# Performance work log

Hardware: AMD Instinct MI355X
Metric: run time of the kernel (lower is better)

## Reference

```python
import jax, jax.numpy as jnp
from jax import lax
import numpy as np

CONF_THRESH = 0.015
NMS_DIST = 4
BORDER = 4
RED = 8


def setup_inputs() -> dict:
    key = jax.random.key(0)
    k1, k2, k3, k4, k5 = jax.random.split(key, 5)
    B, C, H, W = 32, 128, 64, 64
    MID, NCLS = 256, RED * RED + 1
    return {
        "x": jax.random.normal(k1, (B, C, H, W), dtype=jnp.float32),
        "w1": jax.random.normal(k2, (MID, C, 3, 3), dtype=jnp.float32) * 0.05,
        "b1": jax.random.normal(k3, (MID,), dtype=jnp.float32) * 0.05,
        "w2": jax.random.normal(k4, (NCLS, MID, 1, 1), dtype=jnp.float32) * 0.05,
        "b2": jax.random.normal(k5, (NCLS,), dtype=jnp.float32) * 0.05,
    }


def _conv3x3(x, w, b):
    y = lax.conv_general_dilated(
        x, w, window_strides=(1, 1), padding="SAME",
        dimension_numbers=("NCHW", "OIHW", "NCHW"))
    return y + b[None, :, None, None]


def _max_pool(s, r):
    # s: [B, H, W]; infinity-norm neighborhood max, window (2r+1)x(2r+1)
    return lax.reduce_window(
        s, -jnp.inf, lax.max,
        window_dimensions=(1, 2 * r + 1, 2 * r + 1),
        window_strides=(1, 1, 1), padding="SAME")


def _grid_nms(scores, r, iters=8):
    # Iterated local-max suppression; converges to the greedy (sorted-by-score)
    # grid NMS of the original nms_fast routine for distinct scores.
    zeros = jnp.zeros_like(scores)
    max_mask = (scores == _max_pool(scores, r)) & (scores > 0)
    for _ in range(iters):
        supp = _max_pool(max_mask.astype(scores.dtype), r) > 0
        supp_scores = jnp.where(supp, zeros, scores)
        new_max = (supp_scores == _max_pool(supp_scores, r)) & (supp_scores > 0)
        max_mask = max_mask | (new_max & ~supp)
    return jnp.where(max_mask, scores, zeros)


def reference(x, w1, b1, w2, b2):
    B, _, hh, ww = x.shape
    h = jax.nn.relu(_conv3x3(x, w1, b1))                       # [B, mid, hh, ww]
    semi = jnp.einsum("bchw,oc->bohw", h, w2[:, :, 0, 0]) + b2[None, :, None, None]
    dense = jax.nn.softmax(semi, axis=1)                        # [B, 65, hh, ww]
    nodust = dense[:, :-1]                                      # drop dust bin
    # depth-to-space: [B,64,hh,ww] -> [B, hh*8, ww*8]
    heat = nodust.transpose(0, 2, 3, 1).reshape(B, hh, ww, RED, RED)
    heat = heat.transpose(0, 1, 3, 2, 4).reshape(B, hh * RED, ww * RED)
    # confidence threshold
    scores = jnp.where(heat >= CONF_THRESH, heat, 0.0)
    # grid-based NMS (dense keep-map formulation of nms_fast)
    kept = _grid_nms(scores, NMS_DIST)
    # border removal
    Hi, Wi = hh * RED, ww * RED
    yy = jnp.arange(Hi)
    xx = jnp.arange(Wi)
    border = ((yy[:, None] >= BORDER) & (yy[:, None] < Hi - BORDER) &
              (xx[None, :] >= BORDER) & (xx[None, :] < Wi - BORDER))
    return kept * border[None, :, :].astype(kept.dtype)
```

## Files before the change

kernel.cpp:

```cpp
#include <hip/hip_runtime.h>
#include <hip/hip_bf16.h>
#include <stdint.h>

#define BATCH 32
#define CIN 128
#define HH 64
#define WW 64
#define MID 256
#define NCLS 65
#define HI 512
#define NWORDS 8
#define HBS2 264
#define SEMS 68

typedef _Float16 half8 __attribute__((ext_vector_type(8)));
typedef _Float16 half4v __attribute__((ext_vector_type(4)));
typedef _Float16 half2v __attribute__((ext_vector_type(2)));
typedef float f32x4 __attribute__((ext_vector_type(4)));

__global__ __launch_bounds__(256) void prep_w1f(
    const float* __restrict__ w1, _Float16* __restrict__ w1fh,
    _Float16* __restrict__ w1fl)
{
    const int idx = blockIdx.x * 256 + threadIdx.x;
    const int j = idx & 7, lane = (idx >> 3) & 63, mt = (idx >> 9) & 15;
    const int s = (idx >> 13) & 3, kix = idx >> 15;
    const int m = mt * 16 + (lane & 15);
    const int c = s * 32 + (lane >> 4) * 8 + j;
    const int ky = kix / 3, kx = kix - ky * 3;
    const float v = w1[((m * CIN + c) * 3 + ky) * 3 + kx];
    const _Float16 hi = (_Float16)v;
    w1fh[idx] = hi;
    w1fl[idx] = (_Float16)(v - (float)hi);
}

__global__ __launch_bounds__(256) void prep_w2f(
    const float* __restrict__ w2, _Float16* __restrict__ w2fh,
    _Float16* __restrict__ w2fl)
{
    const int idx = blockIdx.x * 256 + threadIdx.x;
    const int j = idx & 7, lane = (idx >> 3) & 63;
    const int ks = (idx >> 9) & 7, mt = idx >> 12;
    const int o = mt * 16 + (lane & 15);
    const int k = ks * 32 + (lane >> 4) * 8 + j;
    const float v = (o < NCLS) ? w2[o * MID + k] : 0.f;
    const _Float16 hi = (_Float16)v;
    w2fh[idx] = hi;
    w2fl[idx] = (_Float16)(v - (float)hi);
}

__global__ __launch_bounds__(256, 3) void head_kernel(
    const float* __restrict__ x,
    const _Float16* __restrict__ w1fh, const _Float16* __restrict__ w1fl,
    const _Float16* __restrict__ w2fh, const _Float16* __restrict__ w2fl,
    const float* __restrict__ b1, const float* __restrict__ b2,
    float* __restrict__ out)
{
    const int b  = blockIdx.z;
    const int y0 = blockIdx.y * 8, x0 = blockIdx.x * 8;
    const int tid = threadIdx.x;
    const int lane = tid & 63, w = tid >> 6;
    const int n = lane & 15, q = lane >> 4;

    __shared__ __align__(16) unsigned char SM[51200];
    char* const xhb = (char*)SM;
    _Float16* const hbh = (_Float16*)SM;
    _Float16* const hbl = hbh + 32 * HBS2;
    float* const sem  = (float*)(SM + 33792);
    float* const rinv = sem + 32 * SEMS;

    const float* xb = x + (size_t)b * CIN * HH * WW;
    for (int i = tid; i < 6400; i += 256) {
        const int c2 = i / 100, pos = i - c2 * 100;
        const int r = pos / 10, cc = pos - r * 10;
        const int gy = y0 - 1 + r, gx = x0 - 1 + cc;
        float v0 = 0.f, v1 = 0.f;
        if ((unsigned)gy < HH && (unsigned)gx < WW) {
            const float* p = xb + (c2 * 2 * HH + gy) * WW + gx;
            v0 = p[0]; v1 = p[HH * WW];
        }
        const _Float16 h0 = (_Float16)v0, h1 = (_Float16)v1;
        half2v hi = {h0, h1};
        half2v lo = {(_Float16)(v0 - (float)h0), (_Float16)(v1 - (float)h1)};
        const int slot = (c2 >> 2) ^ (pos & 15);
        char* p16 = xhb + pos * 256 + (slot << 4) + (c2 & 3) * 4;
        *(half2v*)p16 = hi;
        *(half2v*)(p16 + 25600) = lo;
    }
    __syncthreads();

    f32x4 acc[4][4];
#pragma unroll
    for (int i = 0; i < 4; ++i)
#pragma unroll
        for (int t = 0; t < 4; ++t) acc[i][t] = (f32x4){0.f, 0.f, 0.f, 0.f};

    int bposT[4];
#pragma unroll
    for (int t = 0; t < 4; ++t)
        bposT[t] = (t * 2 + (n >> 3)) * 10 + (n & 7);

    for (int kix = 0; kix < 9; ++kix) {
        const int ky = kix / 3;
        const int koff = ky * 10 + (kix - ky * 3);
#pragma unroll
        for (int s = 0; s < 4; ++s) {
            half8 Bh[4], Bl[4];
#pragma unroll
            for (int t = 0; t < 4; ++t) {
                const int pos = bposT[t] + koff;
                const int byteoff = pos * 256 +
                    ((((s << 2) + q) ^ (pos & 15)) << 4);
                Bh[t] = *(const half8*)(xhb + byteoff);
                Bl[t] = *(const half8*)(xhb + 25600 + byteoff);
            }
#pragma unroll
            for (int i = 0; i < 4; ++i) {
                const size_t o = (size_t)(kix * 4 + s) * 8192 +
                                 (w * 4 + i) * 512 + lane * 8;
                const half8 Ah = *(const half8*)(w1fh + o);
                const half8 Al = *(const half8*)(w1fl + o);
#pragma unroll
                for (int t = 0; t < 4; ++t) {
                    acc[i][t] = __builtin_amdgcn_mfma_f32_16x16x32_f16(
                        Ah, Bh[t], acc[i][t], 0, 0, 0);
                    acc[i][t] = __builtin_amdgcn_mfma_f32_16x16x32_f16(
                        Ah, Bl[t], acc[i][t], 0, 0, 0);
                    acc[i][t] = __builtin_amdgcn_mfma_f32_16x16x32_f16(
                        Al, Bh[t], acc[i][t], 0, 0, 0);
                }
            }
        }
    }
    __syncthreads();

    for (int hf = 0; hf < 2; ++hf) {
        if (hf) __syncthreads();
#pragma unroll
        for (int i = 0; i < 4; ++i)
#pragma unroll
            for (int tt = 0; tt < 2; ++tt) {
                const int t = hf * 2 + tt;
                const int p = tt * 16 + n;
                const int m0 = w * 64 + i * 16 + q * 4;
                const f32x4 a = acc[i][t];
                const float4 bv = *(const float4*)(b1 + m0);
                const float h0 = fmaxf(a[0] + bv.x, 0.f);
                const float h1 = fmaxf(a[1] + bv.y, 0.f);
                const float h2 = fmaxf(a[2] + bv.z, 0.f);
                const float h3 = fmaxf(a[3] + bv.w, 0.f);
                half4v hh = {(_Float16)h0, (_Float16)h1,
                             (_Float16)h2, (_Float16)h3};
                half4v hl = {(_Float16)(h0 - (float)hh[0]),
                             (_Float16)(h1 - (float)hh[1]),
                             (_Float16)(h2 - (float)hh[2]),
                             (_Float16)(h3 - (float)hh[3])};
                *(half4v*)(hbh + p * HBS2 + m0) = hh;
                *(half4v*)(hbl + p * HBS2 + m0) = hl;
            }
        __syncthreads();
        {
            const int nt = w & 1;
            const int mt0 = (w < 2) ? 0 : 3;
            const int nmt = (w < 2) ? 3 : 2;
            const int pb = nt * 16 + n;
            f32x4 a2[3];
#pragma unroll
            for (int j = 0; j < 3; ++j) a2[j] = (f32x4){0.f, 0.f, 0.f, 0.f};
#pragma unroll
            for (int ks = 0; ks < 8; ++ks) {
                const int ad = pb * HBS2 + ks * 32 + q * 8;
                const half8 B2h = *(const half8*)(hbh + ad);
                const half8 B2l = *(const half8*)(hbl + ad);
#pragma unroll
                for (int j = 0; j < 3; ++j)
                    if (j < nmt) {
                        const size_t o = (size_t)((mt0 + j) * 8 + ks) * 512 +
                                         lane * 8;
                        const half8 A2h = *(const half8*)(w2fh + o);
                        const half8 A2l = *(const half8*)(w2fl + o);
                        a2[j] = __builtin_amdgcn_mfma_f32_16x16x32_f16(
                            A2h, B2h, a2[j], 0, 0, 0);
                        a2[j] = __builtin_amdgcn_mfma_f32_16x16x32_f16(
                            A2h, B2l, a2[j], 0, 0, 0);
                        a2[j] = __builtin_amdgcn_mfma_f32_16x16x32_f16(
                            A2l, B2h, a2[j], 0, 0, 0);
                    }
            }
#pragma unroll
            for (int j = 0; j < 3; ++j)
                if (j < nmt) {
                    const int o0 = (mt0 + j) * 16 + q * 4;
#pragma unroll
                    for (int r2 = 0; r2 < 4; ++r2) {
                        const int o = o0 + r2;
                        if (o < NCLS)
                            sem[pb * SEMS + o] = a2[j][r2] + b2[o];
                    }
                }
        }
        __syncthreads();
        if (tid < 128) {
            const int p = tid >> 2, q4 = tid & 3;
            const int o0 = q4 * 17;
            const int o1 = (o0 + 17 < NCLS) ? o0 + 17 : NCLS;
            float mx = -1e30f;
            for (int o = o0; o < o1; ++o)
                mx = fmaxf(mx, sem[p * SEMS + o]);
            mx = fmaxf(mx, __shfl_xor(mx, 1));
            mx = fmaxf(mx, __shfl_xor(mx, 2));
            float ssum = 0.f;
            for (int o = o0; o < o1; ++o) {
                float e = __expf(sem[p * SEMS + o] - mx);
                sem[p * SEMS + o] = e;
                ssum += e;
            }
            ssum += __shfl_xor(ssum, 1);
            ssum += __shfl_xor(ssum, 2);
            if (q4 == 0) rinv[p] = 1.f / ssum;
        }
        __syncthreads();
        for (int t2 = tid; t2 < 2048; t2 += 256) {
            const int p = t2 >> 6, o = t2 & 63;
            float v = sem[p * SEMS + o] * rinv[p];
            if (!(v >= 0.015f)) v = 0.f;
            const int P = hf * 32 + p;
            const int py = P >> 3, px = P & 7;
            const int row = (y0 + py) * 8 + (o >> 3);
            const int col = (x0 + px) * 8 + (o & 7);
            out[((size_t)b * HI + row) * HI + col] = v;
        }
    }
}

__global__ __launch_bounds__(256) void nms_iter(
    const float* __restrict__ S, const uint64_t* __restrict__ Min,
    uint64_t* __restrict__ Mout)
{
    const int b = blockIdx.z;
    const int bx = blockIdx.x;
    const int ty = blockIdx.y * 64, tx = bx * 64;
    const int tid = threadIdx.x;

    __shared__ uint64_t smw[80 * 3];
    __shared__ uint64_t hd[80 * 3];
    __shared__ uint64_t sup[72 * 3];
    __shared__ __align__(16) float sfl[72 * 76];
    __shared__ __align__(16) float rm[40 * 64];

    if (tid < 240) {
        const int i = tid / 3, j = tid % 3;
        const int yy = ty - 8 + i;
        const int wj = bx - 1 + j;
        uint64_t v = 0;
        if (Min && (unsigned)yy < HI && (unsigned)wj < NWORDS)
            v = Min[((size_t)b * HI + yy) * NWORDS + wj];
        smw[tid] = v;
    }
    __syncthreads();
    if (tid < 240) {
        const int i = tid / 3, j = tid % 3;
        const uint64_t c = smw[i * 3 + j];
        const uint64_t l = j > 0 ? smw[i * 3 + j - 1] : 0ull;
        const uint64_t r = j < 2 ? smw[i * 3 + j + 1] : 0ull;
        uint64_t d = c;
#pragma unroll
        for (int s = 1; s <= 4; ++s)
            d |= (c >> s) | (r << (64 - s)) | (c << s) | (l >> (64 - s));
        hd[tid] = d;
    }
    __syncthreads();
    if (tid < 216) {
        const int r = tid / 3, j = tid % 3;
        uint64_t v = 0;
#pragma unroll
        for (int k = 0; k < 9; ++k) v |= hd[(r + k) * 3 + j];
        sup[tid] = v;
    }
    __syncthreads();
    const float* Sb = S + (size_t)b * HI * HI;
    for (int k = tid; k < 72 * 18; k += 256) {
        const int r = k / 18, f4 = k % 18;
        const int gy = ty - 4 + r;
        const int gx0 = tx - 4 + f4 * 4;
        float4 v = make_float4(0.f, 0.f, 0.f, 0.f);
        float* pv = (float*)&v;
        if ((unsigned)gy < HI) {
            if (gx0 >= 0 && gx0 + 3 < HI)
                v = *(const float4*)(Sb + (size_t)gy * HI + gx0);
            else {
#pragma unroll
                for (int cc = 0; cc < 4; ++cc)
                    if ((unsigned)(gx0 + cc) < HI)
                        pv[cc] = Sb[(size_t)gy * HI + gx0 + cc];
            }
        }
        const int rel64 = 60 + 4 * f4;
        const uint64_t w = sup[r * 3 + (rel64 >> 6)];
        const int b0 = rel64 & 63;
#pragma unroll
        for (int cc = 0; cc < 4; ++cc)
            if ((w >> (b0 + cc)) & 1ull) pv[cc] = 0.f;
        *(float4*)(sfl + r * 76 + f4 * 4) = v;
    }
    __syncthreads();

    for (int half = 0; half < 2; ++half) {
        const int rbase = half * 32;
        for (int k = tid; k < 40 * 16; k += 256) {
            const int rr = k / 16, x4 = (k % 16) * 4;
            const int r = rbase + rr;
            const float4 a  = *(const float4*)(sfl + r * 76 + x4);
            const float4 bq = *(const float4*)(sfl + r * 76 + x4 + 4);
            const float4 cq = *(const float4*)(sfl + r * 76 + x4 + 8);
            const float v0=a.x,v1=a.y,v2=a.z,v3=a.w;
            const float v4=bq.x,v5=bq.y,v6=bq.z,v7=bq.w;
            const float v8=cq.x,v9=cq.y,v10=cq.z,v11=cq.w;
            const float m4567 = fmaxf(fmaxf(v4,v5), fmaxf(v6,v7));
            const float m23 = fmaxf(v2,v3), m89 = fmaxf(v8,v9);
            const float o0 = fmaxf(fmaxf(fmaxf(v0,v1), m23), fmaxf(m4567, v8));
            const float o1 = fmaxf(fmaxf(v1, m23), fmaxf(m4567, m89));
            const float o2 = fmaxf(fmaxf(m23, m4567), fmaxf(m89, v10));
            const float o3 = fmaxf(fmaxf(v3, m4567), fmaxf(fmaxf(m89, v10), v11));
            *(float4*)(rm + rr * 64 + x4) = make_float4(o0,o1,o2,o3);
        }
        __syncthreads();
        {
            const int wv = tid >> 6, lane = tid & 63;
            const int rb = wv * 8;
            const int ybase = rbase + rb;
            float ring[9];
#pragma unroll
            for (int k = 0; k < 8; ++k) ring[k] = rm[(rb + k) * 64 + lane];
#pragma unroll
            for (int qq = 0; qq < 8; ++qq) {
                const int y = ybase + qq;
                ring[(qq + 8) % 9] = rm[(rb + qq + 8) * 64 + lane];
                float mv = ring[0];
#pragma unroll
                for (int k = 1; k < 9; ++k) mv = fmaxf(mv, ring[k]);
                const float c = sfl[(y + 4) * 76 + lane + 4];
                const uint64_t oldw = smw[(y + 8) * 3 + 1];
                const bool keep = ((oldw >> lane) & 1ull) || (c == mv && c > 0.f);
                const uint64_t word = __ballot(keep);
                if (lane == 0)
                    Mout[((size_t)b * HI + ty + y) * NWORDS + bx] = word;
            }
        }
        __syncthreads();
    }
}

__global__ __launch_bounds__(256) void finalize_bits(
    float* __restrict__ S, const uint64_t* __restrict__ Mw)
{
    const int i4 = blockIdx.x * 256 + threadIdx.x;
    const size_t base = (size_t)i4 * 4;
    const int x = (int)(base & 511);
    const int y = (int)((base >> 9) & 511);
    const int bb = (int)(base >> 18);
    const uint64_t w = Mw[((size_t)bb * HI + y) * NWORDS + (x >> 6)];
    float4 v = ((const float4*)S)[i4];
    float* pv = (float*)&v;
    const bool rowok = (y >= 4) && (y < HI - 4);
#pragma unroll
    for (int cc = 0; cc < 4; ++cc) {
        const int xx = x + cc;
        const bool keep = rowok && (xx >= 4) && (xx < HI - 4) &&
                          ((w >> (xx & 63)) & 1ull);
        if (!keep) pv[cc] = 0.f;
    }
    ((float4*)S)[i4] = v;
}

extern "C" void kernel_launch(void* const* d_in, const int* in_sizes, int n_in,
                              void* d_out, int out_size, void* d_ws, size_t ws_size,
                              hipStream_t stream) {
    const float* x  = (const float*)d_in[0];
    const float* w1 = (const float*)d_in[1];
    const float* b1 = (const float*)d_in[2];
    const float* w2 = (const float*)d_in[3];
    const float* b2 = (const float*)d_in[4];
    float* out = (float*)d_out;

    char* wsb = (char*)d_ws;
    _Float16* w1fh = (_Float16*)(wsb);
    _Float16* w1fl = (_Float16*)(wsb + 0x90000);
    _Float16* w2fh = (_Float16*)(wsb + 0x120000);
    _Float16* w2fl = (_Float16*)(wsb + 0x130000);
    uint64_t* MA   = (uint64_t*)(wsb + 0x140000);
    uint64_t* MB   = (uint64_t*)(wsb + 0x240000);

    prep_w1f<<<294912 / 256, 256, 0, stream>>>(w1, w1fh, w1fl);
    prep_w2f<<<20480 / 256, 256, 0, stream>>>(w2, w2fh, w2fl);
    head_kernel<<<dim3(8, 8, BATCH), 256, 0, stream>>>(
        x, w1fh, w1fl, w2fh, w2fl, b1, b2, out);

    dim3 g(NWORDS, 8, BATCH);
    nms_iter<<<g, 256, 0, stream>>>(out, nullptr, MA);
    for (int it = 0; it < 4; ++it) {
        nms_iter<<<g, 256, 0, stream>>>(out, MA, MB);
        nms_iter<<<g, 256, 0, stream>>>(out, MB, MA);
    }
    const int nf4 = BATCH * HI * HI / 4;
    finalize_bits<<<nf4 / 256, 256, 0, stream>>>(out, MA);
}
```

Before: 532.4 us.

## Fuse pairs of NMS iterations into one kernel with halo recompute

Adds an nms_pair kernel that performs two suppression iterations per launch. It loads a wider halo tile, computes the intermediate keep mask in shared memory over an enlarged region, then runs the second iteration on the inner tile. The launch sequence drops from nine nms_iter launches to four nms_pair launches plus one nms_iter. This halves global reads of scores and mask words and cuts launch overhead, in exchange for redundant halo computation and more shared memory per block.

```diff
diff --git a/kernel.cpp b/kernel.cpp
--- a/kernel.cpp
+++ b/kernel.cpp
@@ -351,6 +351,240 @@
     }
 }
 
+__global__ __launch_bounds__(256) void nms_pair(
+    const float* __restrict__ S, const uint64_t* __restrict__ Min,
+    uint64_t* __restrict__ Mout)
+{
+    const int b = blockIdx.z;
+    const int bx = blockIdx.x;
+    const int ty = blockIdx.y * 64, tx = bx * 64;
+    const int tid = threadIdx.x;
+
+    __shared__ uint64_t smw[96 * 3];
+    __shared__ uint64_t hd[96 * 3];
+    __shared__ uint64_t sup[88 * 3];
+    __shared__ __align__(16) float sfl[88 * 88];
+    __shared__ __align__(16) float hm[28 * 80];
+    __shared__ uint64_t mkA[80 * 3];
+
+    for (int k = tid; k < 288; k += 256) {
+        const int i = k / 3, j = k - (k / 3) * 3;
+        const int yy = ty - 16 + i;
+        const int wj = bx - 1 + j;
+        uint64_t v = 0;
+        if (Min && (unsigned)yy < HI && (unsigned)wj < NWORDS)
+            v = Min[((size_t)b * HI + yy) * NWORDS + wj];
+        smw[k] = v;
+    }
+    __syncthreads();
+    for (int k = tid; k < 288; k += 256) {
+        const int j = k % 3;
+        const uint64_t c = smw[k];
+        const uint64_t l = j > 0 ? smw[k - 1] : 0ull;
+        const uint64_t r = j < 2 ? smw[k + 1] : 0ull;
+        uint64_t d = c;
+#pragma unroll
+        for (int s = 1; s <= 4; ++s)
+            d |= (c >> s) | (r << (64 - s)) | (c << s) | (l >> (64 - s));
+        hd[k] = d;
+    }
+    __syncthreads();
+    for (int k = tid; k < 264; k += 256) {
+        uint64_t v = 0;
+#pragma unroll
+        for (int t = 0; t < 9; ++t) v |= hd[k + 3 * t];
+        sup[k] = v;
+    }
+    __syncthreads();
+    const float* Sb = S + (size_t)b * HI * HI;
+#pragma unroll
+    for (int u = 0; u < 8; ++u) {
+        const int k = tid + u * 256;
+        if (k < 1936) {
+            const int r = k / 22, f4 = k - r * 22;
+            const int gy = ty - 12 + r;
+            const int gx0 = tx - 12 + f4 * 4;
+            float4 v = make_float4(0.f, 0.f, 0.f, 0.f);
+            float* pv = (float*)&v;
+            if ((unsigned)gy < HI) {
+                if (gx0 >= 0 && gx0 + 3 < HI)
+                    v = *(const float4*)(Sb + (size_t)gy * HI + gx0);
+                else {
+#pragma unroll
+                    for (int cc = 0; cc < 4; ++cc)
+                        if ((unsigned)(gx0 + cc) < HI)
+                            pv[cc] = Sb[(size_t)gy * HI + gx0 + cc];
+                }
+            }
+            const int rel64 = 52 + 4 * f4;
+            const uint64_t w = sup[r * 3 + (rel64 >> 6)];
+            const int b0 = rel64 & 63;
+#pragma unroll
+            for (int cc = 0; cc < 4; ++cc)
+                if ((w >> (b0 + cc)) & 1ull) pv[cc] = 0.f;
+            *(float4*)(sfl + r * 88 + f4 * 4) = v;
+        }
+    }
+    __syncthreads();
+
+    for (int q = 0; q < 4; ++q) {
+#pragma unroll
+        for (int u = 0; u < 3; ++u) {
+            const int k = tid + u * 256;
+            if (k < 560) {
+                const int hr = k / 20, g = k - hr * 20;
+                const int rs = q * 20 + hr;
+                const int cc0 = 4 + 4 * g;
+                const float4 a  = *(const float4*)(sfl + rs * 88 + cc0 - 4);
+                const float4 bq = *(const float4*)(sfl + rs * 88 + cc0);
+                const float4 cq = *(const float4*)(sfl + rs * 88 + cc0 + 4);
+                const float v0=a.x,v1=a.y,v2=a.z,v3=a.w;
+                const float v4=bq.x,v5=bq.y,v6=bq.z,v7=bq.w;
+                const float v8=cq.x,v9=cq.y,v10=cq.z,v11=cq.w;
+                const float m4567 = fmaxf(fmaxf(v4,v5), fmaxf(v6,v7));
+                const float m23 = fmaxf(v2,v3), m89 = fmaxf(v8,v9);
+                const float o0 = fmaxf(fmaxf(fmaxf(v0,v1), m23), fmaxf(m4567, v8));
+                const float o1 = fmaxf(fmaxf(v1, m23), fmaxf(m4567, m89));
+                const float o2 = fmaxf(fmaxf(m23, m4567), fmaxf(m89, v10));
+                const float o3 = fmaxf(fmaxf(v3, m4567), fmaxf(fmaxf(m89, v10), v11));
+                *(float4*)(hm + hr * 80 + 4 * g) = make_float4(o0,o1,o2,o3);
+            }
+        }
+        __syncthreads();
+        {
+            const int wv = tid >> 6, lane = tid & 63;
+            const int kk0 = wv * 5;
+            float ringA[9], ringB[9];
+#pragma unroll
+            for (int t = 0; t < 8; ++t) {
+                ringA[t] = hm[(kk0 + t) * 80 + lane];
+                ringB[t] = (lane < 16) ? hm[(kk0 + t) * 80 + 64 + lane] : 0.f;
+            }
+#pragma unroll
+            for (int i5 = 0; i5 < 5; ++i5) {
+                const int kk = kk0 + i5;
+                ringA[(i5 + 8) % 9] = hm[(kk + 8) * 80 + lane];
+                ringB[(i5 + 8) % 9] =
+                    (lane < 16) ? hm[(kk + 8) * 80 + 64 + lane] : 0.f;
+                float mvA = ringA[0], mvB = ringB[0];
+#pragma unroll
+                for (int t = 1; t < 9; ++t) {
+                    mvA = fmaxf(mvA, ringA[t]);
+                    mvB = fmaxf(mvB, ringB[t]);
+                }
+                const int a = q * 20 + kk;
+                const int rsf = a + 4;
+                const float cA = sfl[rsf * 88 + 4 + lane];
+                const float cB = (lane < 16) ? sfl[rsf * 88 + 68 + lane] : 0.f;
+                const int iw = a + 8;
+                const uint64_t wA = smw[iw * 3 + ((56 + lane) >> 6)];
+                const bool bitA = (wA >> ((56 + lane) & 63)) & 1ull;
+                const uint64_t wB = smw[iw * 3 + ((120 + lane) >> 6)];
+                const bool bitB = (wB >> ((120 + lane) & 63)) & 1ull;
+                const bool keepA = bitA || (cA > 0.f && cA == mvA);
+                const bool keepB =
+                    (lane < 16) && (bitB || (cB > 0.f && cB == mvB));
+                const uint64_t bA = __ballot(keepA);
+                const uint64_t bB = __ballot(keepB);
+                if (lane == 0) {
+                    mkA[a * 3 + 0] = (bA & 0xFFull) << 56;
+                    mkA[a * 3 + 1] = (bA >> 8) | ((bB & 0xFFull) << 56);
+                    mkA[a * 3 + 2] = (bB >> 8) & 0xFFull;
+                }
+            }
+        }
+        __syncthreads();
+    }
+
+    for (int k = tid; k < 240; k += 256) {
+        const int j = k % 3;
+        const uint64_t c = mkA[k];
+        const uint64_t l = j > 0 ? mkA[k - 1] : 0ull;
+        const uint64_t r = j < 2 ? mkA[k + 1] : 0ull;
+        uint64_t d = c;
+#pragma unroll
+        for (int s = 1; s <= 4; ++s)
+            d |= (c >> s) | (r << (64 - s)) | (c << s) | (l >> (64 - s));
+        hd[k] = d;
+    }
+    __syncthreads();
+    for (int k = tid; k < 216; k += 256) {
+        uint64_t v = 0;
+#pragma unroll
+        for (int t = 0; t < 9; ++t) v |= hd[k + 3 * t];
+        sup[k] = v;
+    }
+    __syncthreads();
+#pragma unroll
+    for (int u = 0; u < 6; ++u) {
+        const int k = tid + u * 256;
+        if (k < 1296) {
+            const int r = k / 18, f4 = k - r * 18;
+            const int idx = (r + 8) * 88 + 8 + 4 * f4;
+            float4 v = *(const float4*)(sfl + idx);
+            float* pv = (float*)&v;
+            const int rel64 = 60 + 4 * f4;
+            const uint64_t w = sup[r * 3 + (rel64 >> 6)];
+            const int b0 = rel64 & 63;
+#pragma unroll
+            for (int cc = 0; cc < 4; ++cc)
+                if ((w >> (b0 + cc)) & 1ull) pv[cc] = 0.f;
+            *(float4*)(sfl + idx) = v;
+        }
+    }
+    __syncthreads();
+
+    for (int q = 0; q < 4; ++q) {
+#pragma unroll
+        for (int u = 0; u < 2; ++u) {
+            const int k = tid + u * 256;
+            if (k < 384) {
+                const int hr = k / 16, g = k - hr * 16;
+                const int rs = q * 16 + hr + 8;
+                const int cc0 = 12 + 4 * g;
+                const float4 a  = *(const float4*)(sfl + rs * 88 + cc0 - 4);
+                const float4 bq = *(const float4*)(sfl + rs * 88 + cc0);
+                const float4 cq = *(const float4*)(sfl + rs * 88 + cc0 + 4);
+                const float v0=a.x,v1=a.y,v2=a.z,v3=a.w;
+                const float v4=bq.x,v5=bq.y,v6=bq.z,v7=bq.w;
+                const float v8=cq.x,v9=cq.y,v10=cq.z,v11=cq.w;
+                const float m4567 = fmaxf(fmaxf(v4,v5), fmaxf(v6,v7));
+                const float m23 = fmaxf(v2,v3), m89 = fmaxf(v8,v9);
+                const float o0 = fmaxf(fmaxf(fmaxf(v0,v1), m23), fmaxf(m4567, v8));
+                const float o1 = fmaxf(fmaxf(v1, m23), fmaxf(m4567, m89));
+                const float o2 = fmaxf(fmaxf(m23, m4567), fmaxf(m89, v10));
+                const float o3 = fmaxf(fmaxf(v3, m4567), fmaxf(fmaxf(m89, v10), v11));
+                *(float4*)(hm + hr * 64 + 4 * g) = make_float4(o0,o1,o2,o3);
+            }
+        }
+        __syncthreads();
+        {
+            const int wv = tid >> 6, lane = tid & 63;
+            const int kk0 = wv * 4;
+            float ring[9];
+#pragma unroll
+            for (int t = 0; t < 8; ++t) ring[t] = hm[(kk0 + t) * 64 + lane];
+#pragma unroll
+            for (int i4 = 0; i4 < 4; ++i4) {
+                const int kk = kk0 + i4;
+                ring[(i4 + 8) % 9] = hm[(kk + 8) * 64 + lane];
+                float mv = ring[0];
+#pragma unroll
+                for (int t = 1; t < 9; ++t) mv = fmaxf(mv, ring[t]);
+                const int yo = ty + q * 16 + kk;
+                const float c = sfl[(q * 16 + kk + 12) * 88 + 12 + lane];
+                const int a = q * 16 + kk + 8;
+                const bool bit = (mkA[a * 3 + 1] >> lane) & 1ull;
+                const bool keep = bit || (c > 0.f && c == mv);
+                const uint64_t word = __ballot(keep);
+                if (lane == 0)
+                    Mout[((size_t)b * HI + yo) * NWORDS + bx] = word;
+            }
+        }
+        __syncthreads();
+    }
+}
+
 __global__ __launch_bounds__(256) void finalize_bits(
     float* __restrict__ S, const uint64_t* __restrict__ Mw)
 {
@@ -397,11 +631,12 @@
         x, w1fh, w1fl, w2fh, w2fl, b1, b2, out);
 
     dim3 g(NWORDS, 8, BATCH);
-    nms_iter<<<g, 256, 0, stream>>>(out, nullptr, MA);
-    for (int it = 0; it < 4; ++it) {
-        nms_iter<<<g, 256, 0, stream>>>(out, MA, MB);
-        nms_iter<<<g, 256, 0, stream>>>(out, MB, MA);
-    }
+    nms_pair<<<g, 256, 0, stream>>>(out, nullptr, MA);
+    nms_pair<<<g, 256, 0, stream>>>(out, MA, MB);
+    nms_pair<<<g, 256, 0, stream>>>(out, MB, MA);
+    nms_pair<<<g, 256, 0, stream>>>(out, MA, MB);
+    nms_iter<<<g, 256, 0, stream>>>(out, MB, MA);
+
     const int nf4 = BATCH * HI * HI / 4;
     finalize_bits<<<nf4 / 256, 256, 0, stream>>>(out, MA);
 }
```

Result: slower. 576.0 us (+8.2%).

## Drop shared score tile in NMS iteration, read scores directly from global

Applied to the files above, without the earlier changes.

The NMS iteration kernel no longer stages the 72x76 suppressed-score tile in shared memory. Each thread loads its 12-wide window straight from global memory, applies the suppression mask in registers and writes the horizontal max. The center value is re-read from global in the vertical pass. Launch bounds now request 8 blocks per CU and the row-max buffer gets a padded stride. This cuts LDS use to raise occupancy and removes a barrier, at the cost of overlapping redundant global/L2 reads.

```diff
diff --git a/kernel.cpp b/kernel.cpp
--- a/kernel.cpp
+++ b/kernel.cpp
@@ -12,6 +12,7 @@
 #define NWORDS 8
 #define HBS2 264
 #define SEMS 68
+#define RMS 68
 
 typedef _Float16 half8 __attribute__((ext_vector_type(8)));
 typedef _Float16 half4v __attribute__((ext_vector_type(4)));
@@ -233,7 +234,7 @@
     }
 }
 
-__global__ __launch_bounds__(256) void nms_iter(
+__global__ __launch_bounds__(256, 8) void nms_iter(
     const float* __restrict__ S, const uint64_t* __restrict__ Min,
     uint64_t* __restrict__ Mout)
 {
@@ -245,8 +246,7 @@
     __shared__ uint64_t smw[80 * 3];
     __shared__ uint64_t hd[80 * 3];
     __shared__ uint64_t sup[72 * 3];
-    __shared__ __align__(16) float sfl[72 * 76];
-    __shared__ __align__(16) float rm[40 * 64];
+    __shared__ __align__(16) float rm[40 * RMS];
 
     if (tid < 240) {
         const int i = tid / 3, j = tid % 3;
@@ -259,10 +259,10 @@
     }
     __syncthreads();
     if (tid < 240) {
-        const int i = tid / 3, j = tid % 3;
-        const uint64_t c = smw[i * 3 + j];
-        const uint64_t l = j > 0 ? smw[i * 3 + j - 1] : 0ull;
-        const uint64_t r = j < 2 ? smw[i * 3 + j + 1] : 0ull;
+        const int j = tid % 3;
+        const uint64_t c = smw[tid];
+        const uint64_t l = j > 0 ? smw[tid - 1] : 0ull;
+        const uint64_t r = j < 2 ? smw[tid + 1] : 0ull;
         uint64_t d = c;
 #pragma unroll
         for (int s = 1; s <= 4; ++s)
@@ -271,58 +271,64 @@
     }
     __syncthreads();
     if (tid < 216) {
-        const int r = tid / 3, j = tid % 3;
         uint64_t v = 0;
 #pragma unroll
-        for (int k = 0; k < 9; ++k) v |= hd[(r + k) * 3 + j];
+        for (int k = 0; k < 9; ++k) v |= hd[tid + 3 * k];
         sup[tid] = v;
     }
     __syncthreads();
+
     const float* Sb = S + (size_t)b * HI * HI;
-    for (int k = tid; k < 72 * 18; k += 256) {
-        const int r = k / 18, f4 = k % 18;
-        const int gy = ty - 4 + r;
-        const int gx0 = tx - 4 + f4 * 4;
-        float4 v = make_float4(0.f, 0.f, 0.f, 0.f);
-        float* pv = (float*)&v;
-        if ((unsigned)gy < HI) {
-            if (gx0 >= 0 && gx0 + 3 < HI)
-                v = *(const float4*)(Sb + (size_t)gy * HI + gx0);
-            else {
-#pragma unroll
-                for (int cc = 0; cc < 4; ++cc)
-                    if ((unsigned)(gx0 + cc) < HI)
-                        pv[cc] = Sb[(size_t)gy * HI + gx0 + cc];
-            }
-        }
-        const int rel64 = 60 + 4 * f4;
-        const uint64_t w = sup[r * 3 + (rel64 >> 6)];
-        const int b0 = rel64 & 63;
-#pragma unroll
-        for (int cc = 0; cc < 4; ++cc)
-            if ((w >> (b0 + cc)) & 1ull) pv[cc] = 0.f;
-        *(float4*)(sfl + r * 76 + f4 * 4) = v;
-    }
-    __syncthreads();
-
     for (int half = 0; half < 2; ++half) {
         const int rbase = half * 32;
-        for (int k = tid; k < 40 * 16; k += 256) {
-            const int rr = k / 16, x4 = (k % 16) * 4;
+        for (int k = tid; k < 640; k += 256) {
+            const int rr = k >> 4, g = k & 15;
             const int r = rbase + rr;
-            const float4 a  = *(const float4*)(sfl + r * 76 + x4);
-            const float4 bq = *(const float4*)(sfl + r * 76 + x4 + 4);
-            const float4 cq = *(const float4*)(sfl + r * 76 + x4 + 8);
-            const float v0=a.x,v1=a.y,v2=a.z,v3=a.w;
-            const float v4=bq.x,v5=bq.y,v6=bq.z,v7=bq.w;
-            const float v8=cq.x,v9=cq.y,v10=cq.z,v11=cq.w;
-            const float m4567 = fmaxf(fmaxf(v4,v5), fmaxf(v6,v7));
-            const float m23 = fmaxf(v2,v3), m89 = fmaxf(v8,v9);
-            const float o0 = fmaxf(fmaxf(fmaxf(v0,v1), m23), fmaxf(m4567, v8));
-            const float o1 = fmaxf(fmaxf(v1, m23), fmaxf(m4567, m89));
-            const float o2 = fmaxf(fmaxf(m23, m4567), fmaxf(m89, v10));
-            const float o3 = fmaxf(fmaxf(v3, m4567), fmaxf(fmaxf(m89, v10), v11));
-            *(float4*)(rm + rr * 64 + x4) = make_float4(o0,o1,o2,o3);
+            const int gy = ty - 4 + r;
+            const int x4 = g * 4;
+            const int gx0 = tx + x4 - 4;
+            float v[12];
+            if ((unsigned)gy < HI) {
+                const float* row = Sb + (size_t)gy * HI;
+                if (gx0 >= 0 && gx0 <= HI - 12) {
+                    const float4 A  = *(const float4*)(row + gx0);
+                    const float4 Bq = *(const float4*)(row + gx0 + 4);
+                    const float4 Cq = *(const float4*)(row + gx0 + 8);
+                    v[0]=A.x; v[1]=A.y; v[2]=A.z; v[3]=A.w;
+                    v[4]=Bq.x; v[5]=Bq.y; v[6]=Bq.z; v[7]=Bq.w;
+                    v[8]=Cq.x; v[9]=Cq.y; v[10]=Cq.z; v[11]=Cq.w;
+                } else {
+#pragma unroll
+                    for (int cc = 0; cc < 12; ++cc)
+                        v[cc] = ((unsigned)(gx0 + cc) < HI) ? row[gx0 + cc]
+                                                            : 0.f;
+                }
+            } else {
+#pragma unroll
+                for (int cc = 0; cc < 12; ++cc) v[cc] = 0.f;
+            }
+            const uint64_t* sr = sup + r * 3;
+            const uint64_t w0 = sr[(60 + x4) >> 6];
+            const uint64_t w1 = sr[(64 + x4) >> 6];
+            const uint64_t w2 = sr[(68 + x4) >> 6];
+            const int b0 = (60 + x4) & 63;
+            const int b1 = (64 + x4) & 63;
+            const int b2 = (68 + x4) & 63;
+#pragma unroll
+            for (int cc = 0; cc < 4; ++cc) {
+                if ((w0 >> (b0 + cc)) & 1ull) v[cc] = 0.f;
+                if ((w1 >> (b1 + cc)) & 1ull) v[4 + cc] = 0.f;
+                if ((w2 >> (b2 + cc)) & 1ull) v[8 + cc] = 0.f;
+            }
+            const float m4567 = fmaxf(fmaxf(v[4],v[5]), fmaxf(v[6],v[7]));
+            const float m23 = fmaxf(v[2],v[3]), m89 = fmaxf(v[8],v[9]);
+            const float o0 = fmaxf(fmaxf(fmaxf(v[0],v[1]), m23),
+                                   fmaxf(m4567, v[8]));
+            const float o1 = fmaxf(fmaxf(v[1], m23), fmaxf(m4567, m89));
+            const float o2 = fmaxf(fmaxf(m23, m4567), fmaxf(m89, v[10]));
+            const float o3 = fmaxf(fmaxf(v[3], m4567),
+                                   fmaxf(fmaxf(m89, v[10]), v[11]));
+            *(float4*)(rm + rr * RMS + x4) = make_float4(o0,o1,o2,o3);
         }
         __syncthreads();
         {
@@ -331,17 +337,19 @@
             const int ybase = rbase + rb;
             float ring[9];
 #pragma unroll
-            for (int k = 0; k < 8; ++k) ring[k] = rm[(rb + k) * 64 + lane];
+            for (int k = 0; k < 8; ++k) ring[k] = rm[(rb + k) * RMS + lane];
 #pragma unroll
             for (int qq = 0; qq < 8; ++qq) {
                 const int y = ybase + qq;
-                ring[(qq + 8) % 9] = rm[(rb + qq + 8) * 64 + lane];
+                ring[(qq + 8) % 9] = rm[(rb + qq + 8) * RMS + lane];
                 float mv = ring[0];
 #pragma unroll
                 for (int k = 1; k < 9; ++k) mv = fmaxf(mv, ring[k]);
-                const float c = sfl[(y + 4) * 76 + lane + 4];
+                float c = Sb[(size_t)(ty + y) * HI + tx + lane];
+                if ((sup[(y + 4) * 3 + 1] >> lane) & 1ull) c = 0.f;
                 const uint64_t oldw = smw[(y + 8) * 3 + 1];
-                const bool keep = ((oldw >> lane) & 1ull) || (c == mv && c > 0.f);
+                const bool keep = ((oldw >> lane) & 1ull) ||
+                                  (c > 0.f && c == mv);
                 const uint64_t word = __ballot(keep);
                 if (lane == 0)
                     Mout[((size_t)b * HI + ty + y) * NWORDS + bx] = word;
```

New measurement: 536.0 us. No clear change (+0.7%).
